# Kernel tuning notes

Hardware: AMD Instinct MI355X
Metric: run time of the kernel (lower is better)

## Reference

```python
import jax, jax.numpy as jnp
import numpy as np

D_MODEL = 1024
NUM_HEADS = 16
GROUPS = 4
HEADS_PER_GROUP = NUM_HEADS // GROUPS
D_K = D_MODEL // NUM_HEADS
B, S = 2, 2048


def setup_inputs() -> dict:
    key = jax.random.key(0)
    ks = jax.random.split(key, 10)
    sc = 0.02
    return {
        "x": jax.random.normal(ks[0], (B, S, D_MODEL), dtype=jnp.float32),
        "W_Q": jax.random.normal(ks[1], (D_MODEL, D_MODEL), dtype=jnp.float32) * sc,
        "b_Q": jnp.zeros((D_MODEL,), dtype=jnp.float32),
        "W_K": jax.random.normal(ks[2], (GROUPS, D_MODEL, D_K), dtype=jnp.float32) * sc,
        "b_K": jnp.zeros((GROUPS, D_K), dtype=jnp.float32),
        "W_V": jax.random.normal(ks[3], (GROUPS, D_MODEL, D_K), dtype=jnp.float32) * sc,
        "b_V": jnp.zeros((GROUPS, D_K), dtype=jnp.float32),
        "W_O": jax.random.normal(ks[4], (D_MODEL, D_MODEL), dtype=jnp.float32) * sc,
        "b_O": jnp.zeros((D_MODEL,), dtype=jnp.float32),
    }


def reference(x, W_Q, b_Q, W_K, b_K, W_V, b_V, W_O, b_O):
    b, s, _ = x.shape
    # Q: [b, s, d_model] -> [b, groups, heads_per_group, s, d_k]
    Q = (x @ W_Q + b_Q).reshape(b, s, NUM_HEADS, D_K).transpose(0, 2, 1, 3)
    Q = Q.reshape(b, GROUPS, HEADS_PER_GROUP, s, D_K)
    # Shared K/V per group: [b, groups, s, d_k]
    K = jnp.einsum('bsd,gdk->bgsk', x, W_K) + b_K[None, :, None, :]
    V = jnp.einsum('bsd,gdk->bgsk', x, W_V) + b_V[None, :, None, :]
    # scores: [b, groups, heads_per_group, s, s]
    scores = jnp.einsum('bghsk,bgtk->bghst', Q, K) / jnp.sqrt(jnp.float32(D_K))
    attn = jax.nn.softmax(scores, axis=-1)
    # context: [b, groups, heads_per_group, s, d_k] -> [b, s, d_model]
    ctx = jnp.einsum('bghst,bgtk->bghsk', attn, V)
    ctx = ctx.reshape(b, NUM_HEADS, s, D_K).transpose(0, 2, 1, 3).reshape(b, s, D_MODEL)
    return ctx @ W_O + b_O
```

## Files before the change

kernel.cpp:

```cpp
#include <hip/hip_runtime.h>
#include <cstdint>
#include <cstddef>

typedef short bf16x8 __attribute__((ext_vector_type(8)));
typedef float f32x4 __attribute__((ext_vector_type(4)));

#define DM 1024
#define NHEADS 16
#define NGROUPS 4
#define DK 64
#define BATCH 2
#define SEQ 2048
#define MROWS 4096

#define QB_ELEMS   ((size_t)BATCH*NHEADS*SEQ*DK)
#define KB_ELEMS   ((size_t)BATCH*NGROUPS*SEQ*DK)
#define VT_ELEMS   KB_ELEMS
#define XC_ELEMS   ((size_t)MROWS*DM)
#define WQKV_ELEMS ((size_t)1536*DM)
#define WO_ELEMS   ((size_t)DM*DM)

#define SCL_Q 0.180336880f

__device__ __forceinline__ ushort f2bf(float f) {
    union { float f; uint32_t u; } a; a.f = f;
    uint32_t u = a.u;
    return (ushort)((u + 0x7FFFu + ((u >> 16) & 1u)) >> 16);
}

__device__ __forceinline__ void gll16(const void* g, void* l) {
    __builtin_amdgcn_global_load_lds((const __attribute__((address_space(1))) void*)g,
                                     (__attribute__((address_space(3))) void*)l, 16, 0, 0);
}

__device__ __forceinline__ void transpose_tile(
        const float* __restrict__ src, int src_ld, ushort* __restrict__ dst,
        int r0, int c0, int tid, float (*tl)[65])
{
    const int rr = tid >> 4, cc = (tid & 15) * 4;
#pragma unroll
    for (int p = 0; p < 4; p++) {
        int r = rr + p * 16;
        float4 v = *(const float4*)(src + (size_t)(r0 + r) * src_ld + c0 + cc);
        tl[cc + 0][r] = v.x; tl[cc + 1][r] = v.y;
        tl[cc + 2][r] = v.z; tl[cc + 3][r] = v.w;
    }
    __syncthreads();
#pragma unroll
    for (int p = 0; p < 4; p++) {
        int c = rr + p * 16;
        ushort4 o;
        o.x = f2bf(tl[c][cc + 0]); o.y = f2bf(tl[c][cc + 1]);
        o.z = f2bf(tl[c][cc + 2]); o.w = f2bf(tl[c][cc + 3]);
        *(ushort4*)(dst + (size_t)(c0 + c) * 1024 + r0 + cc) = o;
    }
}

__global__ __launch_bounds__(256) void gqa_prep_kernel(
        const float* __restrict__ x,
        const float* __restrict__ WQ, const float* __restrict__ WK,
        const float* __restrict__ WV, const float* __restrict__ WO,
        const float* __restrict__ bQ, const float* __restrict__ bK,
        const float* __restrict__ bV,
        ushort* __restrict__ xbf, ushort* __restrict__ WqkvT,
        ushort* __restrict__ WoT, float* __restrict__ bcat)
{
    __shared__ float tl[64][65];
    const int tid = threadIdx.x;
    for (int u = blockIdx.x; u < 897; u += 512) {
        if (u < 256) {
            transpose_tile(WQ, 1024, WqkvT, (u >> 4) * 64, (u & 15) * 64, tid, tl);
        } else if (u < 320) {
            int t = u - 256, g = t >> 4;
            transpose_tile(WK + (size_t)g * 65536, 64,
                           WqkvT + (size_t)(1024 + g * 64) * 1024,
                           (t & 15) * 64, 0, tid, tl);
        } else if (u < 384) {
            int t = u - 320, g = t >> 4;
            transpose_tile(WV + (size_t)g * 65536, 64,
                           WqkvT + (size_t)(1280 + g * 64) * 1024,
                           (t & 15) * 64, 0, tid, tl);
        } else if (u < 640) {
            int t = u - 384;
            transpose_tile(WO, 1024, WoT, (t >> 4) * 64, (t & 15) * 64, tid, tl);
        } else if (u < 896) {
            int cid = u - 640;
            const float* xs = x + (size_t)cid * 16384;
            ushort* xd = xbf + (size_t)cid * 16384;
#pragma unroll
            for (int p = 0; p < 16; p++) {
                float4 v = *(const float4*)(xs + p * 1024 + tid * 4);
                ushort4 o = { f2bf(v.x), f2bf(v.y), f2bf(v.z), f2bf(v.w) };
                *(ushort4*)(xd + p * 1024 + tid * 4) = o;
            }
        } else {
            for (int k = tid; k < 1536; k += 256) {
                float v = (k < 1024) ? bQ[k] : (k < 1280 ? bK[k - 1024] : bV[k - 1280]);
                bcat[k] = v;
            }
        }
        __syncthreads();
    }
}

template<int NJ, bool QKV_EPI>
__global__ __launch_bounds__(256, 2) void gqa_gemm_kernel(
        const ushort* __restrict__ A, const ushort* __restrict__ BT,
        const float* __restrict__ bias, float* __restrict__ outF,
        ushort* __restrict__ Qb, ushort* __restrict__ Kb,
        ushort* __restrict__ Vtg)
{
    constexpr int BNT = NJ * 32;
    __shared__ ushort smem[16384 + NJ * 4096];
    ushort* As = smem;
    ushort* Bs = smem + 16384;

    const int tid = threadIdx.x;
    const int i = blockIdx.x;
    const int xcd = i & 7, slot = i >> 3;
    const int bm = (slot >> 4) * 8 + xcd;
    const int bn = slot & 15;
    const int wave = tid >> 6, lane = tid & 63;
    const int wm = (wave & 1) * 64, wn = (wave >> 1) * (NJ * 16);
    const int lr = lane & 15, lq = lane >> 4;
    const int swz = lr & 7;

    const ushort* srcA[4]; int dstOffA[4];
    const ushort* srcB[NJ]; int dstOffB[NJ];
#pragma unroll
    for (int p = 0; p < 4; p++) {
        int slt = p * 256 + tid;
        int row = slt >> 3, cb = (slt & 7) ^ (row & 7);
        srcA[p] = A + (size_t)(bm * 128 + row) * 1024 + cb * 8;
        dstOffA[p] = p * 2048 + wave * 512;
    }
#pragma unroll
    for (int p = 0; p < NJ; p++) {
        int slt = p * 256 + tid;
        int row = slt >> 3, cb = (slt & 7) ^ (row & 7);
        srcB[p] = BT + (size_t)(bn * BNT + row) * 1024 + cb * 8;
        dstOffB[p] = p * 2048 + wave * 512;
    }

    f32x4 acc[4][NJ];
#pragma unroll
    for (int ii = 0; ii < 4; ii++)
#pragma unroll
        for (int j = 0; j < NJ; j++) acc[ii][j] = (f32x4){0.f, 0.f, 0.f, 0.f};

#pragma unroll
    for (int p = 0; p < 4; p++) gll16(srcA[p], &As[dstOffA[p]]);
#pragma unroll
    for (int p = 0; p < NJ; p++) gll16(srcB[p], &Bs[dstOffB[p]]);

    for (int kt = 0; kt < 16; kt++) {
        __syncthreads();
        if (kt < 15) {
            int buf = (kt + 1) & 1, ko = (kt + 1) * 64;
#pragma unroll
            for (int p = 0; p < 4; p++)
                gll16(srcA[p] + ko, &As[buf * 8192 + dstOffA[p]]);
#pragma unroll
            for (int p = 0; p < NJ; p++)
                gll16(srcB[p] + ko, &Bs[buf * (NJ * 2048) + dstOffB[p]]);
        }
        const ushort* as = As + (kt & 1) * 8192;
        const ushort* bs = Bs + (kt & 1) * (NJ * 2048);
        bf16x8 af[2][4], bfr[2][NJ];
#pragma unroll
        for (int kh = 0; kh < 2; kh++) {
#pragma unroll
            for (int ii = 0; ii < 4; ii++)
                af[kh][ii] = *(const bf16x8*)&as[(wm + ii * 16 + lr) * 64 + ((kh * 4 + lq) ^ swz) * 8];
#pragma unroll
            for (int j = 0; j < NJ; j++)
                bfr[kh][j] = *(const bf16x8*)&bs[(wn + j * 16 + lr) * 64 + ((kh * 4 + lq) ^ swz) * 8];
        }
#pragma unroll
        for (int kh = 0; kh < 2; kh++)
#pragma unroll
            for (int ii = 0; ii < 4; ii++)
#pragma unroll
                for (int j = 0; j < NJ; j++)
                    acc[ii][j] = __builtin_amdgcn_mfma_f32_16x16x32_bf16(af[kh][ii], bfr[kh][j], acc[ii][j], 0, 0, 0);
    }

#pragma unroll
    for (int ii = 0; ii < 4; ii++) {
        int mg = bm * 128 + wm + ii * 16 + lq * 4;
        int b = mg >> 11, s = mg & 2047;
#pragma unroll
        for (int j = 0; j < NJ; j++) {
            int cg = bn * BNT + wn + j * 16 + lr;
            float bv = bias[cg];
            if constexpr (QKV_EPI) {
                int d = cg & 63;
                if (cg < 1024) {
                    int h = cg >> 6;
                    ushort* dst = Qb + ((size_t)(b * NHEADS + h) * SEQ + s) * DK + d;
#pragma unroll
                    for (int r = 0; r < 4; r++)
                        dst[r * DK] = f2bf((acc[ii][j][r] + bv) * SCL_Q);
                } else if (cg < 1280) {
                    int g = (cg - 1024) >> 6;
                    ushort* dst = Kb + ((size_t)(b * NGROUPS + g) * SEQ + s) * DK + d;
#pragma unroll
                    for (int r = 0; r < 4; r++) dst[r * DK] = f2bf(acc[ii][j][r] + bv);
                } else {
                    int g = (cg - 1280) >> 6;
                    int s4 = s >> 2, kg = s4 & 7;
                    int col = ((s4 >> 3) << 5) + (((((kg & 3) << 1) | (kg >> 2))) << 2);
                    ushort4 pk;
                    pk.x = f2bf(acc[ii][j][0] + bv); pk.y = f2bf(acc[ii][j][1] + bv);
                    pk.z = f2bf(acc[ii][j][2] + bv); pk.w = f2bf(acc[ii][j][3] + bv);
                    *(ushort4*)(Vtg + ((size_t)(b * NGROUPS + g) * DK + d) * SEQ + col) = pk;
                }
            } else {
#pragma unroll
                for (int r = 0; r < 4; r++)
                    outF[(size_t)(mg + r) * DM + cg] = acc[ii][j][r] + bv;
            }
        }
    }
}

__global__ __launch_bounds__(256, 2) void gqa_attn_kernel(
        const ushort* __restrict__ Qb, const ushort* __restrict__ Kb,
        const ushort* __restrict__ Vtg, ushort* __restrict__ ctx)
{
    __shared__ ushort Ks[2][128 * 64];
    __shared__ ushort Vs[2][64 * 128];

    const int tid = threadIdx.x, wave = tid >> 6, lane = tid & 63;
    const int lr = lane & 15, lq = lane >> 4;
    const int swz = lr & 7;
    const int wq = wave & 1, wt = wave >> 1;
    const int i = blockIdx.x;
    const int bg = i & 7, s2 = i >> 3;
    const int qt = s2 & 15, h = s2 >> 4;
    const int b = bg >> 2, g = bg & 3, hg = g * 4 + h;

    const ushort* Qh = Qb  + (size_t)(b * NHEADS  + hg) * SEQ * DK;
    const ushort* Kg = Kb  + (size_t)(b * NGROUPS + g)  * SEQ * DK;
    const ushort* Vg = Vtg + (size_t)(b * NGROUPS + g)  * DK * SEQ;

    const int s0 = qt * 128 + wq * 64;
    const int tb = wt * 64;

    bf16x8 qf[4][2];
#pragma unroll
    for (int qs = 0; qs < 4; qs++)
#pragma unroll
        for (int kh = 0; kh < 2; kh++)
            qf[qs][kh] = *(const bf16x8*)(Qh + (size_t)(s0 + qs * 16 + lr) * DK + kh * 32 + lq * 8);

    const ushort* srcK[4]; const ushort* srcV[4]; int dstOff[4];
#pragma unroll
    for (int p = 0; p < 4; p++) {
        int slt = p * 256 + tid;
        int krow = slt >> 3, kcb = (slt & 7) ^ (krow & 7);
        srcK[p] = Kg + (size_t)krow * DK + kcb * 8;
        int vrow = slt >> 4, vc = slt & 15;
        int vcb = (vc & 8) | ((vc ^ vrow) & 7);
        srcV[p] = Vg + (size_t)vrow * SEQ + vcb * 8;
        dstOff[p] = (p * 256 + wave * 64) * 8;
    }

    f32x4 of[4][4];
#pragma unroll
    for (int qs = 0; qs < 4; qs++)
#pragma unroll
        for (int j = 0; j < 4; j++) of[qs][j] = (f32x4){0.f, 0.f, 0.f, 0.f};
    f32x4 accL[4];
#pragma unroll
    for (int qs = 0; qs < 4; qs++) accL[qs] = (f32x4){0.f, 0.f, 0.f, 0.f};

    bf16x8 ones;
#pragma unroll
    for (int k = 0; k < 8; k++) ones[k] = (short)0x3F80;

#pragma unroll
    for (int p = 0; p < 4; p++) {
        gll16(srcK[p], &Ks[0][dstOff[p]]);
        gll16(srcV[p], &Vs[0][dstOff[p]]);
    }

    for (int it = 0; it < 16; it++) {
        __syncthreads();
        if (it < 15) {
            int buf = (it + 1) & 1, t0 = (it + 1) * 128;
#pragma unroll
            for (int p = 0; p < 4; p++) {
                gll16(srcK[p] + (size_t)t0 * DK, &Ks[buf][dstOff[p]]);
                gll16(srcV[p] + t0, &Vs[buf][dstOff[p]]);
            }
        }
        const ushort* ks = Ks[it & 1];
        const ushort* vs = Vs[it & 1];

        bf16x8 kf[4][2];
#pragma unroll
        for (int nt = 0; nt < 4; nt++)
#pragma unroll
            for (int kh = 0; kh < 2; kh++)
                kf[nt][kh] = *(const bf16x8*)&ks[(tb + nt * 16 + lr) * 64 + ((kh * 4 + lq) ^ swz) * 8];

        bf16x8 vf[4][2];
#pragma unroll
        for (int j = 0; j < 4; j++)
#pragma unroll
            for (int kk = 0; kk < 2; kk++)
                vf[j][kk] = *(const bf16x8*)&vs[(j * 16 + lr) * 128 + (wt * 8 + ((kk * 4 + lq) ^ swz)) * 8];

        f32x4 sc[4][4];
#pragma unroll
        for (int qs = 0; qs < 4; qs++)
#pragma unroll
            for (int nt = 0; nt < 4; nt++) {
                f32x4 s = (f32x4){0.f, 0.f, 0.f, 0.f};
                s = __builtin_amdgcn_mfma_f32_16x16x32_bf16(kf[nt][0], qf[qs][0], s, 0, 0, 0);
                s = __builtin_amdgcn_mfma_f32_16x16x32_bf16(kf[nt][1], qf[qs][1], s, 0, 0, 0);
                sc[qs][nt] = s;
            }

        union PF { bf16x8 v; uint32_t w[4]; };
        PF pf[4][2];
#pragma unroll
        for (int qs = 0; qs < 4; qs++) {
#pragma unroll
            for (int nt = 0; nt < 4; nt++) {
                union { float f; uint32_t u; } e0, e1, e2, e3;
                e0.f = __builtin_amdgcn_exp2f(sc[qs][nt][0]);
                e1.f = __builtin_amdgcn_exp2f(sc[qs][nt][1]);
                e2.f = __builtin_amdgcn_exp2f(sc[qs][nt][2]);
                e3.f = __builtin_amdgcn_exp2f(sc[qs][nt][3]);
                pf[qs][nt >> 1].w[(nt & 1) * 2 + 0] = __builtin_amdgcn_perm(e1.u, e0.u, 0x07060302u);
                pf[qs][nt >> 1].w[(nt & 1) * 2 + 1] = __builtin_amdgcn_perm(e3.u, e2.u, 0x07060302u);
            }
            accL[qs] = __builtin_amdgcn_mfma_f32_16x16x32_bf16(ones, pf[qs][0].v, accL[qs], 0, 0, 0);
            accL[qs] = __builtin_amdgcn_mfma_f32_16x16x32_bf16(ones, pf[qs][1].v, accL[qs], 0, 0, 0);
        }

#pragma unroll
        for (int qs = 0; qs < 4; qs++)
#pragma unroll
            for (int j = 0; j < 4; j++) {
                of[qs][j] = __builtin_amdgcn_mfma_f32_16x16x32_bf16(vf[j][0], pf[qs][0].v, of[qs][j], 0, 0, 0);
                of[qs][j] = __builtin_amdgcn_mfma_f32_16x16x32_bf16(vf[j][1], pf[qs][1].v, of[qs][j], 0, 0, 0);
            }
    }

    __syncthreads();
    float* comb = (float*)&Ks[0][0];
    float* accX = (float*)&Vs[0][0];
    if (wt == 1) {
        float* cw = comb + wq * 4096;
#pragma unroll
        for (int qs = 0; qs < 4; qs++)
#pragma unroll
            for (int j = 0; j < 4; j++)
                *(f32x4*)&cw[(qs * 4 + j) * 256 + lane * 4] = of[qs][j];
        if (lq == 0) {
#pragma unroll
            for (int qs = 0; qs < 4; qs++) accX[(wq * 4 + qs) * 16 + lr] = accL[qs][0];
        }
    }
    __syncthreads();
    if (wt == 0) {
        const float* cw = comb + wq * 4096;
        float inv[4];
#pragma unroll
        for (int qs = 0; qs < 4; qs++)
            inv[qs] = 1.0f / (accL[qs][0] + accX[(wq * 4 + qs) * 16 + lr]);
        ushort* cbp = ctx + (size_t)b * SEQ * DM;
#pragma unroll
        for (int qs = 0; qs < 4; qs++) {
            int s = s0 + qs * 16 + lr;
#pragma unroll
            for (int j = 0; j < 4; j++) {
                f32x4 o2 = of[qs][j] + *(const f32x4*)&cw[(qs * 4 + j) * 256 + lane * 4];
                ushort4 o;
                o.x = f2bf(o2[0] * inv[qs]);
                o.y = f2bf(o2[1] * inv[qs]);
                o.z = f2bf(o2[2] * inv[qs]);
                o.w = f2bf(o2[3] * inv[qs]);
                *(ushort4*)(cbp + (size_t)s * DM + hg * 64 + j * 16 + lq * 4) = o;
            }
        }
    }
}

extern "C" void kernel_launch(void* const* d_in, const int* in_sizes, int n_in,
                              void* d_out, int out_size, void* d_ws, size_t ws_size,
                              hipStream_t stream) {
    const float* x  = (const float*)d_in[0];
    const float* WQ = (const float*)d_in[1];
    const float* bQ = (const float*)d_in[2];
    const float* WK = (const float*)d_in[3];
    const float* bK = (const float*)d_in[4];
    const float* WV = (const float*)d_in[5];
    const float* bV = (const float*)d_in[6];
    const float* WO = (const float*)d_in[7];
    const float* bO = (const float*)d_in[8];

    ushort* Qb    = (ushort*)d_ws;
    ushort* Kb    = Qb + QB_ELEMS;
    ushort* Vtg   = Kb + KB_ELEMS;
    ushort* xc    = Vtg + VT_ELEMS;
    ushort* WqkvT = xc + XC_ELEMS;
    ushort* WoT   = WqkvT + WQKV_ELEMS;
    float*  bcat  = (float*)(WoT + WO_ELEMS);

    gqa_prep_kernel<<<512, 256, 0, stream>>>(x, WQ, WK, WV, WO, bQ, bK, bV,
                                             xc, WqkvT, WoT, bcat);
    gqa_gemm_kernel<3, true><<<512, 256, 0, stream>>>(
        xc, WqkvT, bcat, nullptr, Qb, Kb, Vtg);
    gqa_attn_kernel<<<512, 256, 0, stream>>>(Qb, Kb, Vtg, xc);
    gqa_gemm_kernel<2, false><<<512, 256, 0, stream>>>(
        xc, WoT, bO, (float*)d_out, nullptr, nullptr, nullptr);
}
```

Baseline: 161.4 us.

## Split attention key tiles across eight waves with four-way partial reduction

The attention kernel grows from 4 to 8 waves per block. Each wave now processes 32 keys of each 128-key tile instead of 64, and the partial outputs and row sums are reduced across four key-slices through shared memory in two stages. s_setprio is wrapped around the MFMA sections, and the launch bound asks for 4 blocks of 512 threads. The aim is more waves in flight to hide LDS and exp latency. The cost is extra reduction traffic and barriers in the epilogue, and register pressure from the tighter bound.

```diff
diff --git a/kernel.cpp b/kernel.cpp
--- a/kernel.cpp
+++ b/kernel.cpp
@@ -224,7 +224,7 @@
     }
 }
 
-__global__ __launch_bounds__(256, 2) void gqa_attn_kernel(
+__global__ __launch_bounds__(512, 4) void gqa_attn_kernel(
         const ushort* __restrict__ Qb, const ushort* __restrict__ Kb,
         const ushort* __restrict__ Vtg, ushort* __restrict__ ctx)
 {
@@ -245,7 +245,7 @@
     const ushort* Vg = Vtg + (size_t)(b * NGROUPS + g)  * DK * SEQ;
 
     const int s0 = qt * 128 + wq * 64;
-    const int tb = wt * 64;
+    const int tb = wt * 32;
 
     bf16x8 qf[4][2];
 #pragma unroll
@@ -254,16 +254,16 @@
         for (int kh = 0; kh < 2; kh++)
             qf[qs][kh] = *(const bf16x8*)(Qh + (size_t)(s0 + qs * 16 + lr) * DK + kh * 32 + lq * 8);
 
-    const ushort* srcK[4]; const ushort* srcV[4]; int dstOff[4];
-#pragma unroll
-    for (int p = 0; p < 4; p++) {
-        int slt = p * 256 + tid;
+    const ushort* srcK[2]; const ushort* srcV[2]; int dstOff[2];
+#pragma unroll
+    for (int p = 0; p < 2; p++) {
+        int slt = p * 512 + tid;
         int krow = slt >> 3, kcb = (slt & 7) ^ (krow & 7);
         srcK[p] = Kg + (size_t)krow * DK + kcb * 8;
         int vrow = slt >> 4, vc = slt & 15;
         int vcb = (vc & 8) | ((vc ^ vrow) & 7);
         srcV[p] = Vg + (size_t)vrow * SEQ + vcb * 8;
-        dstOff[p] = (p * 256 + wave * 64) * 8;
+        dstOff[p] = (p * 512 + wave * 64) * 8;
     }
 
     f32x4 of[4][4];
@@ -280,7 +280,7 @@
     for (int k = 0; k < 8; k++) ones[k] = (short)0x3F80;
 
 #pragma unroll
-    for (int p = 0; p < 4; p++) {
+    for (int p = 0; p < 2; p++) {
         gll16(srcK[p], &Ks[0][dstOff[p]]);
         gll16(srcV[p], &Vs[0][dstOff[p]]);
     }
@@ -290,7 +290,7 @@
         if (it < 15) {
             int buf = (it + 1) & 1, t0 = (it + 1) * 128;
 #pragma unroll
-            for (int p = 0; p < 4; p++) {
+            for (int p = 0; p < 2; p++) {
                 gll16(srcK[p] + (size_t)t0 * DK, &Ks[buf][dstOff[p]]);
                 gll16(srcV[p] + t0, &Vs[buf][dstOff[p]]);
             }
@@ -298,80 +298,109 @@
         const ushort* ks = Ks[it & 1];
         const ushort* vs = Vs[it & 1];
 
-        bf16x8 kf[4][2];
-#pragma unroll
-        for (int nt = 0; nt < 4; nt++)
+        bf16x8 kf[2][2];
+#pragma unroll
+        for (int nt = 0; nt < 2; nt++)
 #pragma unroll
             for (int kh = 0; kh < 2; kh++)
                 kf[nt][kh] = *(const bf16x8*)&ks[(tb + nt * 16 + lr) * 64 + ((kh * 4 + lq) ^ swz) * 8];
 
-        bf16x8 vf[4][2];
-#pragma unroll
-        for (int j = 0; j < 4; j++)
-#pragma unroll
-            for (int kk = 0; kk < 2; kk++)
-                vf[j][kk] = *(const bf16x8*)&vs[(j * 16 + lr) * 128 + (wt * 8 + ((kk * 4 + lq) ^ swz)) * 8];
-
-        f32x4 sc[4][4];
-#pragma unroll
-        for (int qs = 0; qs < 4; qs++)
-#pragma unroll
-            for (int nt = 0; nt < 4; nt++) {
+        bf16x8 vf[4];
+        {
+            int gch = wt * 4 + lq;
+            int vc2 = (gch & 8) | ((gch ^ swz) & 7);
+#pragma unroll
+            for (int j = 0; j < 4; j++)
+                vf[j] = *(const bf16x8*)&vs[(j * 16 + lr) * 128 + vc2 * 8];
+        }
+
+        f32x4 sc[4][2];
+        __builtin_amdgcn_s_setprio(1);
+#pragma unroll
+        for (int qs = 0; qs < 4; qs++)
+#pragma unroll
+            for (int nt = 0; nt < 2; nt++) {
                 f32x4 s = (f32x4){0.f, 0.f, 0.f, 0.f};
                 s = __builtin_amdgcn_mfma_f32_16x16x32_bf16(kf[nt][0], qf[qs][0], s, 0, 0, 0);
                 s = __builtin_amdgcn_mfma_f32_16x16x32_bf16(kf[nt][1], qf[qs][1], s, 0, 0, 0);
                 sc[qs][nt] = s;
             }
+        __builtin_amdgcn_s_setprio(0);
 
         union PF { bf16x8 v; uint32_t w[4]; };
-        PF pf[4][2];
-#pragma unroll
-        for (int qs = 0; qs < 4; qs++) {
-#pragma unroll
-            for (int nt = 0; nt < 4; nt++) {
+        PF pf[4];
+#pragma unroll
+        for (int qs = 0; qs < 4; qs++)
+#pragma unroll
+            for (int nt = 0; nt < 2; nt++) {
                 union { float f; uint32_t u; } e0, e1, e2, e3;
                 e0.f = __builtin_amdgcn_exp2f(sc[qs][nt][0]);
                 e1.f = __builtin_amdgcn_exp2f(sc[qs][nt][1]);
                 e2.f = __builtin_amdgcn_exp2f(sc[qs][nt][2]);
                 e3.f = __builtin_amdgcn_exp2f(sc[qs][nt][3]);
-                pf[qs][nt >> 1].w[(nt & 1) * 2 + 0] = __builtin_amdgcn_perm(e1.u, e0.u, 0x07060302u);
-                pf[qs][nt >> 1].w[(nt & 1) * 2 + 1] = __builtin_amdgcn_perm(e3.u, e2.u, 0x07060302u);
-            }
-            accL[qs] = __builtin_amdgcn_mfma_f32_16x16x32_bf16(ones, pf[qs][0].v, accL[qs], 0, 0, 0);
-            accL[qs] = __builtin_amdgcn_mfma_f32_16x16x32_bf16(ones, pf[qs][1].v, accL[qs], 0, 0, 0);
-        }
-
-#pragma unroll
-        for (int qs = 0; qs < 4; qs++)
-#pragma unroll
-            for (int j = 0; j < 4; j++) {
-                of[qs][j] = __builtin_amdgcn_mfma_f32_16x16x32_bf16(vf[j][0], pf[qs][0].v, of[qs][j], 0, 0, 0);
-                of[qs][j] = __builtin_amdgcn_mfma_f32_16x16x32_bf16(vf[j][1], pf[qs][1].v, of[qs][j], 0, 0, 0);
-            }
+                pf[qs].w[nt * 2 + 0] = __builtin_amdgcn_perm(e1.u, e0.u, 0x07060302u);
+                pf[qs].w[nt * 2 + 1] = __builtin_amdgcn_perm(e3.u, e2.u, 0x07060302u);
+            }
+
+        __builtin_amdgcn_s_setprio(1);
+#pragma unroll
+        for (int qs = 0; qs < 4; qs++)
+            accL[qs] = __builtin_amdgcn_mfma_f32_16x16x32_bf16(ones, pf[qs].v, accL[qs], 0, 0, 0);
+#pragma unroll
+        for (int qs = 0; qs < 4; qs++)
+#pragma unroll
+            for (int j = 0; j < 4; j++)
+                of[qs][j] = __builtin_amdgcn_mfma_f32_16x16x32_bf16(vf[j], pf[qs].v, of[qs][j], 0, 0, 0);
+        __builtin_amdgcn_s_setprio(0);
     }
 
     __syncthreads();
-    float* comb = (float*)&Ks[0][0];
-    float* accX = (float*)&Vs[0][0];
-    if (wt == 1) {
-        float* cw = comb + wq * 4096;
+    float* combA = (float*)&Ks[0][0];
+    float* combB = (float*)&Vs[0][0];
+    if (wt >= 2) {
+        float* cw = (wq * 2 + (wt - 2)) < 2 ? combA + (wq * 2 + (wt - 2)) * 4096
+                                            : combB + (wq * 2 + (wt - 2) - 2) * 4096;
 #pragma unroll
         for (int qs = 0; qs < 4; qs++)
 #pragma unroll
             for (int j = 0; j < 4; j++)
                 *(f32x4*)&cw[(qs * 4 + j) * 256 + lane * 4] = of[qs][j];
-        if (lq == 0) {
-#pragma unroll
-            for (int qs = 0; qs < 4; qs++) accX[(wq * 4 + qs) * 16 + lr] = accL[qs][0];
-        }
+    }
+    __syncthreads();
+    if (wt < 2) {
+        const float* cw = (wq * 2 + wt) < 2 ? combA + (wq * 2 + wt) * 4096
+                                            : combB + (wq * 2 + wt - 2) * 4096;
+#pragma unroll
+        for (int qs = 0; qs < 4; qs++)
+#pragma unroll
+            for (int j = 0; j < 4; j++)
+                of[qs][j] += *(const f32x4*)&cw[(qs * 4 + j) * 256 + lane * 4];
+    }
+    __syncthreads();
+    float* accXs = combB;
+    if (wt == 1) {
+        float* cw = combA + wq * 4096;
+#pragma unroll
+        for (int qs = 0; qs < 4; qs++)
+#pragma unroll
+            for (int j = 0; j < 4; j++)
+                *(f32x4*)&cw[(qs * 4 + j) * 256 + lane * 4] = of[qs][j];
+    }
+    if (lq == 0) {
+#pragma unroll
+        for (int qs = 0; qs < 4; qs++)
+            accXs[wave * 64 + qs * 16 + lr] = accL[qs][0];
     }
     __syncthreads();
     if (wt == 0) {
-        const float* cw = comb + wq * 4096;
+        const float* cw = combA + wq * 4096;
         float inv[4];
 #pragma unroll
         for (int qs = 0; qs < 4; qs++)
-            inv[qs] = 1.0f / (accL[qs][0] + accX[(wq * 4 + qs) * 16 + lr]);
+            inv[qs] = 1.0f / (accXs[(wq) * 64 + qs * 16 + lr]
+                            + accXs[(wq + 2) * 64 + qs * 16 + lr]
+                            + accXs[(wq + 4) * 64 + qs * 16 + lr]
+                            + accXs[(wq + 6) * 64 + qs * 16 + lr]);
         ushort* cbp = ctx + (size_t)b * SEQ * DM;
 #pragma unroll
         for (int qs = 0; qs < 4; qs++) {
@@ -415,7 +444,7 @@
                                              xc, WqkvT, WoT, bcat);
     gqa_gemm_kernel<3, true><<<512, 256, 0, stream>>>(
         xc, WqkvT, bcat, nullptr, Qb, Kb, Vtg);
-    gqa_attn_kernel<<<512, 256, 0, stream>>>(Qb, Kb, Vtg, xc);
+    gqa_attn_kernel<<<512, 512, 0, stream>>>(Qb, Kb, Vtg, xc);
     gqa_gemm_kernel<2, false><<<512, 256, 0, stream>>>(
         xc, WoT, bO, (float*)d_out, nullptr, nullptr, nullptr);
 }
```

Result: slower. 365.5 us (+126.4%).

## Load K/V fragments directly from global memory instead of LDS double-buffering

Applied to the files above, without the earlier changes.

The attention kernel no longer stages K and V tiles through double-buffered shared memory with per-iteration barriers. Each wave now loads its MFMA K and V fragments straight from global memory (relying on L2/L1 for reuse across waves). s_setprio is also raised around the MFMA sections. This removes the barriers and the LDS traffic, but gives up the explicit prefetch and adds redundant global loads across the waves that share the same K/V.

```diff
diff --git a/kernel.cpp b/kernel.cpp
--- a/kernel.cpp
+++ b/kernel.cpp
@@ -228,12 +228,11 @@
         const ushort* __restrict__ Qb, const ushort* __restrict__ Kb,
         const ushort* __restrict__ Vtg, ushort* __restrict__ ctx)
 {
-    __shared__ ushort Ks[2][128 * 64];
-    __shared__ ushort Vs[2][64 * 128];
+    __shared__ float comb[2][4096];
+    __shared__ float accX[128];
 
     const int tid = threadIdx.x, wave = tid >> 6, lane = tid & 63;
     const int lr = lane & 15, lq = lane >> 4;
-    const int swz = lr & 7;
     const int wq = wave & 1, wt = wave >> 1;
     const int i = blockIdx.x;
     const int bg = i & 7, s2 = i >> 3;
@@ -254,18 +253,6 @@
         for (int kh = 0; kh < 2; kh++)
             qf[qs][kh] = *(const bf16x8*)(Qh + (size_t)(s0 + qs * 16 + lr) * DK + kh * 32 + lq * 8);
 
-    const ushort* srcK[4]; const ushort* srcV[4]; int dstOff[4];
-#pragma unroll
-    for (int p = 0; p < 4; p++) {
-        int slt = p * 256 + tid;
-        int krow = slt >> 3, kcb = (slt & 7) ^ (krow & 7);
-        srcK[p] = Kg + (size_t)krow * DK + kcb * 8;
-        int vrow = slt >> 4, vc = slt & 15;
-        int vcb = (vc & 8) | ((vc ^ vrow) & 7);
-        srcV[p] = Vg + (size_t)vrow * SEQ + vcb * 8;
-        dstOff[p] = (p * 256 + wave * 64) * 8;
-    }
-
     f32x4 of[4][4];
 #pragma unroll
     for (int qs = 0; qs < 4; qs++)
@@ -279,40 +266,29 @@
 #pragma unroll
     for (int k = 0; k < 8; k++) ones[k] = (short)0x3F80;
 
-#pragma unroll
-    for (int p = 0; p < 4; p++) {
-        gll16(srcK[p], &Ks[0][dstOff[p]]);
-        gll16(srcV[p], &Vs[0][dstOff[p]]);
-    }
+    const ushort* kbase = Kg + (size_t)(tb + lr) * DK + lq * 8;
+    const ushort* vbase = Vg + (size_t)lr * SEQ + wt * 64 + lq * 8;
 
     for (int it = 0; it < 16; it++) {
-        __syncthreads();
-        if (it < 15) {
-            int buf = (it + 1) & 1, t0 = (it + 1) * 128;
-#pragma unroll
-            for (int p = 0; p < 4; p++) {
-                gll16(srcK[p] + (size_t)t0 * DK, &Ks[buf][dstOff[p]]);
-                gll16(srcV[p] + t0, &Vs[buf][dstOff[p]]);
-            }
-        }
-        const ushort* ks = Ks[it & 1];
-        const ushort* vs = Vs[it & 1];
+        const ushort* kp = kbase + (size_t)it * 128 * DK;
+        const ushort* vp = vbase + it * 128;
 
         bf16x8 kf[4][2];
 #pragma unroll
         for (int nt = 0; nt < 4; nt++)
 #pragma unroll
             for (int kh = 0; kh < 2; kh++)
-                kf[nt][kh] = *(const bf16x8*)&ks[(tb + nt * 16 + lr) * 64 + ((kh * 4 + lq) ^ swz) * 8];
+                kf[nt][kh] = *(const bf16x8*)(kp + (size_t)nt * 16 * DK + kh * 32);
 
         bf16x8 vf[4][2];
 #pragma unroll
         for (int j = 0; j < 4; j++)
 #pragma unroll
             for (int kk = 0; kk < 2; kk++)
-                vf[j][kk] = *(const bf16x8*)&vs[(j * 16 + lr) * 128 + (wt * 8 + ((kk * 4 + lq) ^ swz)) * 8];
+                vf[j][kk] = *(const bf16x8*)(vp + (size_t)j * 16 * SEQ + kk * 32);
 
         f32x4 sc[4][4];
+        __builtin_amdgcn_s_setprio(1);
 #pragma unroll
         for (int qs = 0; qs < 4; qs++)
 #pragma unroll
@@ -322,6 +298,7 @@
                 s = __builtin_amdgcn_mfma_f32_16x16x32_bf16(kf[nt][1], qf[qs][1], s, 0, 0, 0);
                 sc[qs][nt] = s;
             }
+        __builtin_amdgcn_s_setprio(0);
 
         union PF { bf16x8 v; uint32_t w[4]; };
         PF pf[4][2];
@@ -337,10 +314,14 @@
                 pf[qs][nt >> 1].w[(nt & 1) * 2 + 0] = __builtin_amdgcn_perm(e1.u, e0.u, 0x07060302u);
                 pf[qs][nt >> 1].w[(nt & 1) * 2 + 1] = __builtin_amdgcn_perm(e3.u, e2.u, 0x07060302u);
             }
+        }
+
+        __builtin_amdgcn_s_setprio(1);
+#pragma unroll
+        for (int qs = 0; qs < 4; qs++) {
             accL[qs] = __builtin_amdgcn_mfma_f32_16x16x32_bf16(ones, pf[qs][0].v, accL[qs], 0, 0, 0);
             accL[qs] = __builtin_amdgcn_mfma_f32_16x16x32_bf16(ones, pf[qs][1].v, accL[qs], 0, 0, 0);
         }
-
 #pragma unroll
         for (int qs = 0; qs < 4; qs++)
 #pragma unroll
@@ -348,13 +329,12 @@
                 of[qs][j] = __builtin_amdgcn_mfma_f32_16x16x32_bf16(vf[j][0], pf[qs][0].v, of[qs][j], 0, 0, 0);
                 of[qs][j] = __builtin_amdgcn_mfma_f32_16x16x32_bf16(vf[j][1], pf[qs][1].v, of[qs][j], 0, 0, 0);
             }
+        __builtin_amdgcn_s_setprio(0);
     }
 
     __syncthreads();
-    float* comb = (float*)&Ks[0][0];
-    float* accX = (float*)&Vs[0][0];
     if (wt == 1) {
-        float* cw = comb + wq * 4096;
+        float* cw = &comb[wq][0];
 #pragma unroll
         for (int qs = 0; qs < 4; qs++)
 #pragma unroll
@@ -367,7 +347,7 @@
     }
     __syncthreads();
     if (wt == 0) {
-        const float* cw = comb + wq * 4096;
+        const float* cw = &comb[wq][0];
         float inv[4];
 #pragma unroll
         for (int qs = 0; qs < 4; qs++)
```

Result: slower. 184.7 us (+14.4%).
